# Kernel tuning notes

Measured on AMD Instinct MI355X. Metric: run time of the kernel, lower is better.

## Reference

```python
import jax, jax.numpy as jnp
import numpy as np

B, S, D_MODEL, HEADS = 4, 2048, 1024, 16
D = D_MODEL // HEADS  # 64


def setup_inputs() -> dict:
    key = jax.random.key(0)
    ks = jax.random.split(key, 12)
    s = 0.02
    return {
        "query": jax.random.normal(ks[0], (B, S, D_MODEL), jnp.float32),
        "key": jax.random.normal(ks[1], (B, S, D_MODEL), jnp.float32),
        "value": jax.random.normal(ks[2], (B, S, D_MODEL), jnp.float32),
        "mask": jnp.ones((B, 1, S, S), jnp.int32),
        "Wq": jax.random.normal(ks[3], (D, D), jnp.float32) * s,
        "bq": jnp.zeros((D,), jnp.float32),
        "Wk": jax.random.normal(ks[4], (D, D), jnp.float32) * s,
        "bk": jnp.zeros((D,), jnp.float32),
        "Wv": jax.random.normal(ks[5], (D, D), jnp.float32) * s,
        "bv": jnp.zeros((D,), jnp.float32),
        "Wo": jax.random.normal(ks[6], (D_MODEL, HEADS * D), jnp.float32) * s,
        "bo": jnp.zeros((D_MODEL,), jnp.float32),
    }


def reference(query, key, value, mask, Wq, bq, Wk, bk, Wv, bv, Wo, bo):
    b, sq, _ = query.shape
    sk = key.shape[1]
    # split heads: [B, S, H, D]
    q = query.reshape(b, sq, HEADS, D)
    k = key.reshape(b, sk, HEADS, D)
    v = value.reshape(b, sk, HEADS, D)
    # per-head linear projections (weights shared across heads), torch Linear: x @ W.T + b
    q = q @ Wq.T + bq
    k = k @ Wk.T + bk
    v = v @ Wv.T + bv
    # scores [B, H, Sq, Sk]
    score = jnp.einsum("bqhd,bkhd->bhqk", q, k)
    # NOTE: original torch code calls score.masked_fill(...) without assignment
    # (non-in-place, result discarded), so the mask has NO effect. Faithful: skip it.
    # NOTE: scaling is score / (d ** 1 / 2) == score / (d / 2), NOT score / sqrt(d).
    attn = jax.nn.softmax(score / (D / 2.0), axis=-1)
    out = jnp.einsum("bhqk,bkhd->bqhd", attn, v)
    out = out.reshape(b, sq, HEADS * D)
    return out @ Wo.T + bo
```

## Files before the change

### kernel.cpp

```cpp
#include <hip/hip_runtime.h>
#include <hip/hip_bf16.h>

#define B_   4
#define S_   2048
#define H_   16
#define D_   64
#define DM_  1024
#define BH_  (B_ * H_)

#define LOG2E_D32 0.04508422002778011f

typedef unsigned short u16;
typedef u16  u16x4  __attribute__((ext_vector_type(4)));
typedef u16  u16x8  __attribute__((ext_vector_type(8)));
typedef float f32x4 __attribute__((ext_vector_type(4)));
typedef __bf16 bf16x8 __attribute__((ext_vector_type(8)));

__device__ __forceinline__ u16 f2bf(float f) {
    __hip_bfloat16 h = __float2bfloat16(f);
    return *reinterpret_cast<u16*>(&h);
}
__device__ __forceinline__ bf16x8 cvt8(const float* p) {
    float4 a = *(const float4*)p;
    float4 b = *(const float4*)(p + 4);
    u16x8 r;
    r[0] = f2bf(a.x); r[1] = f2bf(a.y); r[2] = f2bf(a.z); r[3] = f2bf(a.w);
    r[4] = f2bf(b.x); r[5] = f2bf(b.y); r[6] = f2bf(b.z); r[7] = f2bf(b.w);
    union { u16x8 u; bf16x8 h; } cv; cv.u = r; return cv.h;
}
__device__ __forceinline__ void load_lds16(const u16* g, u16* l) {
    __builtin_amdgcn_global_load_lds(
        (const __attribute__((address_space(1))) unsigned int*)g,
        (__attribute__((address_space(3))) unsigned int*)l, 16, 0, 0);
}
#define MFMA16(a, b, c) __builtin_amdgcn_mfma_f32_16x16x32_bf16(a, b, c, 0, 0, 0)

__global__ __launch_bounds__(256) void cvt_kernel(
    const float* __restrict__ in, u16* __restrict__ outp)
{
    int i = (blockIdx.x * 256 + threadIdx.x) * 4;
    float4 v = *(const float4*)(in + i);
    u16x4 o; o[0] = f2bf(v.x); o[1] = f2bf(v.y); o[2] = f2bf(v.z); o[3] = f2bf(v.w);
    *(u16x4*)(outp + i) = o;
}

__global__ __launch_bounds__(256) void proj_kernel(
    const float* __restrict__ xq, const float* __restrict__ xk, const float* __restrict__ xv,
    const float* __restrict__ Wq, const float* __restrict__ bq,
    const float* __restrict__ Wk, const float* __restrict__ bk,
    const float* __restrict__ Wv, const float* __restrict__ bv,
    u16* __restrict__ Qp, u16* __restrict__ Kp, u16* __restrict__ Vp)
{
    __shared__ u16 vt[64 * 72];

    const int z     = blockIdx.z;
    const float* x    = (z == 0) ? xq : (z == 1) ? xk : xv;
    const float* W    = (z == 0) ? Wq : (z == 1) ? Wk : Wv;
    const float* bias = (z == 0) ? bq : (z == 1) ? bk : bv;
    const float scale = (z == 0) ? LOG2E_D32 : 1.0f;

    const int tid = threadIdx.x, w = tid >> 6, lane = tid & 63;
    const int l15 = lane & 15, quad = lane >> 4;
    const int bh = blockIdx.y, b = bh >> 4, h = bh & 15;
    const int s0 = blockIdx.x * 64;

    const int srow = s0 + w * 16 + l15;
    const float* xp = x + ((size_t)(b * S_ + srow) * H_ + h) * D_;
    bf16x8 a0 = cvt8(xp + quad * 8);
    bf16x8 a1 = cvt8(xp + 32 + quad * 8);

    f32x4 acc[4];
#pragma unroll
    for (int nt = 0; nt < 4; ++nt) {
        const float* wp = W + (nt * 16 + l15) * D_;
        f32x4 c = {0.f, 0.f, 0.f, 0.f};
        c = MFMA16(a0, cvt8(wp + quad * 8), c);
        c = MFMA16(a1, cvt8(wp + 32 + quad * 8), c);
        acc[nt] = c;
    }

    if (z < 2) {
        u16* out = (z == 0) ? Qp : Kp;
#pragma unroll
        for (int nt = 0; nt < 4; ++nt) {
            float bs = bias[nt * 16 + l15];
#pragma unroll
            for (int r = 0; r < 4; ++r) {
                int sl = w * 16 + quad * 4 + r;
                vt[sl * 72 + nt * 16 + l15] = f2bf((acc[nt][r] + bs) * scale);
            }
        }
        __syncthreads();
#pragma unroll
        for (int u = 0; u < 2; ++u) {
            int sl = (tid >> 3) + u * 32;
            int c  = tid & 7;
            u16x8 val = *(const u16x8*)&vt[sl * 72 + c * 8];
            *(u16x8*)(out + ((size_t)bh * S_ + s0 + sl) * D_ + c * 8) = val;
        }
    } else {
#pragma unroll
        for (int nt = 0; nt < 4; ++nt) {
            float bs = bias[nt * 16 + l15];
            u16x4 pu;
#pragma unroll
            for (int r = 0; r < 4; ++r) pu[r] = f2bf(acc[nt][r] + bs);
            int d  = nt * 16 + l15;
            int cc = w * 16 + quad * 4;
            int ch = (cc >> 3) ^ (d & 7);
            *(u16x4*)&vt[d * 72 + ch * 8 + (cc & 7)] = pu;
        }
        __syncthreads();
        int d  = tid >> 2;
        int cb = (tid & 3) * 16;
        size_t gbase = ((size_t)bh * 64 + d) * S_ + s0;
#pragma unroll
        for (int u = 0; u < 2; ++u) {
            int ch  = (cb >> 3) + u;
            int ch2 = ch ^ (d & 7);
            u16x8 val = *(const u16x8*)&vt[d * 72 + ch2 * 8];
            *(u16x8*)(Vp + gbase + ch * 8) = val;
        }
    }
}

__global__ __launch_bounds__(256, 3) void attn_kernel(
    const u16* __restrict__ Qp, const u16* __restrict__ Kp,
    const u16* __restrict__ Vp, u16* __restrict__ Ao)
{
    __shared__ u16 kt[2][64 * 64];
    __shared__ u16 vt[2][64 * 64];

    const int tid = threadIdx.x, w = tid >> 6, lane = tid & 63;
    const int l15 = lane & 15, quad = lane >> 4;

    const int f = blockIdx.x;
    const int xcd = f & 7, kk = f >> 3;
    const int qtile = kk & 15;
    const int bh = ((kk >> 4) << 3) | xcd;
    const int b = bh >> 4, h = bh & 15;
    const int qbase = qtile * 128 + w * 32;

    bf16x8 qf[2][2];
#pragma unroll
    for (int nt = 0; nt < 2; ++nt) {
        const bf16x8* qp = (const bf16x8*)(Qp + ((size_t)bh * S_ + qbase + nt * 16 + l15) * D_);
        qf[nt][0] = qp[quad];
        qf[nt][1] = qp[4 + quad];
    }

    f32x4 ot[4][2];
#pragma unroll
    for (int mt = 0; mt < 4; ++mt)
#pragma unroll
        for (int nt = 0; nt < 2; ++nt) ot[mt][nt] = (f32x4){0.f, 0.f, 0.f, 0.f};
    float li[2] = {0.f, 0.f};

    const size_t krow = (size_t)bh * S_;
    const size_t vrow = (size_t)bh * 64;

    const int srcA = ((quad & 1) << 5) | l15;
    const int srcB = srcA | 16;
    const bool hi  = quad >= 2;

    auto stage = [&](int it, int buf) {
        const int k0 = it * 64;
#pragma unroll
        for (int c = 0; c < 4; ++c) {
            int ci = w * 4 + c;
            if (ci < 8) {
                int chunk = ci * 64 + lane;
                int r = chunk >> 3, j = chunk & 7;
                load_lds16(Kp + (krow + k0 + r) * D_ + ((j ^ (r & 7)) << 3),
                           &kt[buf][ci * 512]);
            } else {
                int ci2 = ci - 8;
                int chunk = ci2 * 64 + lane;
                int r = chunk >> 3, j = chunk & 7;
                load_lds16(Vp + (vrow + r) * S_ + k0 + ((j ^ (r & 7)) << 3),
                           &vt[buf][ci2 * 512]);
            }
        }
    };

    stage(0, 0);

    for (int it = 0; it < S_ / 64; ++it) {
        const int p = it & 1;
        __syncthreads();

        bf16x8 ak[4][2], av[4][2];
#pragma unroll
        for (int mt = 0; mt < 4; ++mt) {
            int rk = mt * 16 + l15;
            ak[mt][0] = *(const bf16x8*)&kt[p][rk * 64 + ((quad       ^ (rk & 7)) << 3)];
            ak[mt][1] = *(const bf16x8*)&kt[p][rk * 64 + (((4 + quad) ^ (rk & 7)) << 3)];
            av[mt][0] = *(const bf16x8*)&vt[p][rk * 64 + ((quad       ^ (rk & 7)) << 3)];
            av[mt][1] = *(const bf16x8*)&vt[p][rk * 64 + (((4 + quad) ^ (rk & 7)) << 3)];
        }

        if (it + 1 < S_ / 64) stage(it + 1, p ^ 1);

        f32x4 st[4][2];
#pragma unroll
        for (int mt = 0; mt < 4; ++mt)
#pragma unroll
            for (int nt = 0; nt < 2; ++nt) {
                f32x4 c = {0.f, 0.f, 0.f, 0.f};
                c = MFMA16(ak[mt][0], qf[nt][0], c);
                c = MFMA16(ak[mt][1], qf[nt][1], c);
                st[mt][nt] = c;
            }

        uint2 pd[2][4];
#pragma unroll
        for (int nt = 0; nt < 2; ++nt) {
            float s = 0.f;
#pragma unroll
            for (int mt = 0; mt < 4; ++mt) {
                float e0 = __builtin_amdgcn_exp2f(st[mt][nt][0]);
                float e1 = __builtin_amdgcn_exp2f(st[mt][nt][1]);
                float e2 = __builtin_amdgcn_exp2f(st[mt][nt][2]);
                float e3 = __builtin_amdgcn_exp2f(st[mt][nt][3]);
                s += (e0 + e1) + (e2 + e3);
                union { u16x4 v; uint2 d; } pu;
                pu.v[0] = f2bf(e0); pu.v[1] = f2bf(e1);
                pu.v[2] = f2bf(e2); pu.v[3] = f2bf(e3);
                pd[nt][mt] = pu.d;
            }
            li[nt] += s;
        }

#pragma unroll
        for (int ks = 0; ks < 2; ++ks) {
            bf16x8 bp[2];
#pragma unroll
            for (int nt = 0; nt < 2; ++nt) {
                uint2 e0 = pd[nt][2 * ks], e1 = pd[nt][2 * ks + 1];
                int a0x = __shfl((int)e0.x, srcA), a0y = __shfl((int)e0.y, srcA);
                int a1x = __shfl((int)e1.x, srcA), a1y = __shfl((int)e1.y, srcA);
                int b0x = __shfl((int)e0.x, srcB), b0y = __shfl((int)e0.y, srcB);
                int b1x = __shfl((int)e1.x, srcB), b1y = __shfl((int)e1.y, srcB);
                union { uint4 u; bf16x8 h; } cv;
                cv.u.x = (unsigned)(hi ? a1x : a0x);
                cv.u.y = (unsigned)(hi ? a1y : a0y);
                cv.u.z = (unsigned)(hi ? b1x : b0x);
                cv.u.w = (unsigned)(hi ? b1y : b0y);
                bp[nt] = cv.h;
            }
#pragma unroll
            for (int mt = 0; mt < 4; ++mt)
#pragma unroll
                for (int nt = 0; nt < 2; ++nt)
                    ot[mt][nt] = MFMA16(av[mt][ks], bp[nt], ot[mt][nt]);
        }
    }

#pragma unroll
    for (int nt = 0; nt < 2; ++nt) {
        float l = li[nt];
        l += __shfl_xor(l, 16);
        l += __shfl_xor(l, 32);
        float inv = 1.f / l;
        int qrow = qbase + nt * 16 + l15;
        u16* orow = Ao + (((size_t)b * S_ + qrow) * H_ + h) * D_;
#pragma unroll
        for (int mt = 0; mt < 4; ++mt) {
            u16x4 o;
#pragma unroll
            for (int r = 0; r < 4; ++r) o[r] = f2bf(ot[mt][nt][r] * inv);
            *(u16x4*)(orow + mt * 16 + quad * 4) = o;
        }
    }
}

__global__ __launch_bounds__(256) void oproj_kernel(
    const u16* __restrict__ A, const u16* __restrict__ Wob,
    const float* __restrict__ bo, float* __restrict__ C)
{
    __shared__ u16 at[128 * 64];
    __shared__ u16 bt[128 * 64];

    const int tid = threadIdx.x, w = tid >> 6, lane = tid & 63;
    const int l15 = lane & 15, quad = lane >> 4;
    const int m0 = blockIdx.y * 128;
    const int n0 = blockIdx.x * 128;
    const int wm = w & 1, wn = w >> 1;

    f32x4 acc[4][4];
#pragma unroll
    for (int mt = 0; mt < 4; ++mt)
#pragma unroll
        for (int nt = 0; nt < 4; ++nt) acc[mt][nt] = (f32x4){0.f, 0.f, 0.f, 0.f};

    for (int kk = 0; kk < DM_ / 64; ++kk) {
        __syncthreads();
#pragma unroll
        for (int c = 0; c < 8; ++c) {
            int ci = w * 8 + c;
            int t  = ci & 15;
            int chunk = t * 64 + lane;
            int r = chunk >> 3, j = chunk & 7;
            int col = kk * 64 + ((j ^ (r & 7)) << 3);
            if (ci < 16) load_lds16(A   + (size_t)(m0 + r) * DM_ + col, &at[t * 512]);
            else         load_lds16(Wob + (size_t)(n0 + r) * DM_ + col, &bt[t * 512]);
        }
        __syncthreads();

#pragma unroll
        for (int ks = 0; ks < 2; ++ks) {
            bf16x8 af[4], bf[4];
#pragma unroll
            for (int mt = 0; mt < 4; ++mt) {
                int r = wm * 64 + mt * 16 + l15;
                af[mt] = *(const bf16x8*)&at[r * 64 + (((ks * 4 + quad) ^ (r & 7)) << 3)];
            }
#pragma unroll
            for (int nt = 0; nt < 4; ++nt) {
                int r = wn * 64 + nt * 16 + l15;
                bf[nt] = *(const bf16x8*)&bt[r * 64 + (((ks * 4 + quad) ^ (r & 7)) << 3)];
            }
#pragma unroll
            for (int mt = 0; mt < 4; ++mt)
#pragma unroll
                for (int nt = 0; nt < 4; ++nt)
                    acc[mt][nt] = MFMA16(af[mt], bf[nt], acc[mt][nt]);
        }
    }

#pragma unroll
    for (int nt = 0; nt < 4; ++nt) {
        int ng = n0 + wn * 64 + nt * 16 + l15;
        float bs = bo[ng];
#pragma unroll
        for (int mt = 0; mt < 4; ++mt) {
            int mg = m0 + wm * 64 + mt * 16 + quad * 4;
#pragma unroll
            for (int r = 0; r < 4; ++r)
                C[(size_t)(mg + r) * DM_ + ng] = acc[mt][nt][r] + bs;
        }
    }
}

extern "C" void kernel_launch(void* const* d_in, const int* in_sizes, int n_in,
                              void* d_out, int out_size, void* d_ws, size_t ws_size,
                              hipStream_t stream)
{
    const float* q   = (const float*)d_in[0];
    const float* k   = (const float*)d_in[1];
    const float* v   = (const float*)d_in[2];
    const float* Wq  = (const float*)d_in[4];
    const float* bq  = (const float*)d_in[5];
    const float* Wk  = (const float*)d_in[6];
    const float* bk  = (const float*)d_in[7];
    const float* Wv  = (const float*)d_in[8];
    const float* bv  = (const float*)d_in[9];
    const float* Wo  = (const float*)d_in[10];
    const float* bo  = (const float*)d_in[11];
    float* out = (float*)d_out;

    const size_t TENS = (size_t)B_ * S_ * DM_;
    u16* Qp  = (u16*)d_ws;
    u16* Kp  = Qp + TENS;
    u16* Vp  = Kp + TENS;
    u16* Ao  = Vp + TENS;
    u16* Wob = Ao + TENS;

    cvt_kernel<<<dim3((DM_ * DM_) / 1024), 256, 0, stream>>>(Wo, Wob);
    proj_kernel<<<dim3(S_ / 64, BH_, 3), 256, 0, stream>>>(
        q, k, v, Wq, bq, Wk, bk, Wv, bv, Qp, Kp, Vp);
    attn_kernel<<<dim3((S_ / 128) * BH_), 256, 0, stream>>>(Qp, Kp, Vp, Ao);
    oproj_kernel<<<dim3(DM_ / 128, (B_ * S_) / 128), 256, 0, stream>>>(Ao, Wob, bo, out);
}
```

Baseline: 367.9 us.

## Switch attention to 32x32x16 MFMA with larger per-wave query tiles

```diff
diff --git a/kernel.cpp b/kernel.cpp
--- a/kernel.cpp
+++ b/kernel.cpp
@@ -14,6 +14,7 @@
 typedef u16  u16x4  __attribute__((ext_vector_type(4)));
 typedef u16  u16x8  __attribute__((ext_vector_type(8)));
 typedef float f32x4 __attribute__((ext_vector_type(4)));
+typedef float f32x16 __attribute__((ext_vector_type(16)));
 typedef __bf16 bf16x8 __attribute__((ext_vector_type(8)));
 
 __device__ __forceinline__ u16 f2bf(float f) {
@@ -34,6 +35,7 @@
         (__attribute__((address_space(3))) unsigned int*)l, 16, 0, 0);
 }
 #define MFMA16(a, b, c) __builtin_amdgcn_mfma_f32_16x16x32_bf16(a, b, c, 0, 0, 0)
+#define MFMA32(a, b, c) __builtin_amdgcn_mfma_f32_32x32x16_bf16(a, b, c, 0, 0, 0)
 
 __global__ __launch_bounds__(256) void cvt_kernel(
     const float* __restrict__ in, u16* __restrict__ outp)
@@ -124,61 +126,56 @@
     }
 }
 
-__global__ __launch_bounds__(256, 3) void attn_kernel(
+__global__ __launch_bounds__(256, 2) void attn_kernel(
     const u16* __restrict__ Qp, const u16* __restrict__ Kp,
     const u16* __restrict__ Vp, u16* __restrict__ Ao)
 {
-    __shared__ u16 kt[2][64 * 64];
-    __shared__ u16 vt[2][64 * 64];
+    __shared__ u16 kt[2][8 * 64 * 8];
+    __shared__ u16 vt[2][8 * 64 * 8];
 
     const int tid = threadIdx.x, w = tid >> 6, lane = tid & 63;
-    const int l15 = lane & 15, quad = lane >> 4;
+    const int l31 = lane & 31, h = lane >> 5;
 
     const int f = blockIdx.x;
-    const int xcd = f & 7, kk = f >> 3;
-    const int qtile = kk & 15;
-    const int bh = ((kk >> 4) << 3) | xcd;
-    const int b = bh >> 4, h = bh & 15;
-    const int qbase = qtile * 128 + w * 32;
-
-    bf16x8 qf[2][2];
-#pragma unroll
-    for (int nt = 0; nt < 2; ++nt) {
-        const bf16x8* qp = (const bf16x8*)(Qp + ((size_t)bh * S_ + qbase + nt * 16 + l15) * D_);
-        qf[nt][0] = qp[quad];
-        qf[nt][1] = qp[4 + quad];
-    }
-
-    f32x4 ot[4][2];
-#pragma unroll
-    for (int mt = 0; mt < 4; ++mt)
-#pragma unroll
-        for (int nt = 0; nt < 2; ++nt) ot[mt][nt] = (f32x4){0.f, 0.f, 0.f, 0.f};
-    float li[2] = {0.f, 0.f};
+    const int xcd = f & 7;
+    const int g8 = f >> 3;
+    const int qtile = g8 & 7;
+    const int bh = ((g8 >> 3) << 3) | xcd;
+    const int b = bh >> 4, hh = bh & 15;
+    const int qwb = qtile * 256 + w * 64;
 
     const size_t krow = (size_t)bh * S_;
     const size_t vrow = (size_t)bh * 64;
 
-    const int srcA = ((quad & 1) << 5) | l15;
-    const int srcB = srcA | 16;
-    const bool hi  = quad >= 2;
+    bf16x8 qf[2][4];
+#pragma unroll
+    for (int nt = 0; nt < 2; ++nt)
+#pragma unroll
+        for (int kd = 0; kd < 4; ++kd)
+            qf[nt][kd] = *(const bf16x8*)(
+                Qp + ((size_t)bh * S_ + qwb + nt * 32 + l31) * D_ + kd * 16 + h * 8);
+
+    f32x16 ot[2][2];
+#pragma unroll
+    for (int dm = 0; dm < 2; ++dm)
+#pragma unroll
+        for (int nt = 0; nt < 2; ++nt)
+#pragma unroll
+            for (int r = 0; r < 16; ++r) ot[dm][nt][r] = 0.f;
+    float li[2] = {0.f, 0.f};
 
     auto stage = [&](int it, int buf) {
         const int k0 = it * 64;
 #pragma unroll
         for (int c = 0; c < 4; ++c) {
             int ci = w * 4 + c;
-            if (ci < 8) {
-                int chunk = ci * 64 + lane;
-                int r = chunk >> 3, j = chunk & 7;
-                load_lds16(Kp + (krow + k0 + r) * D_ + ((j ^ (r & 7)) << 3),
+            if (ci < 8)
+                load_lds16(Kp + (krow + k0 + lane) * D_ + ci * 8,
                            &kt[buf][ci * 512]);
-            } else {
-                int ci2 = ci - 8;
-                int chunk = ci2 * 64 + lane;
-                int r = chunk >> 3, j = chunk & 7;
-                load_lds16(Vp + (vrow + r) * S_ + k0 + ((j ^ (r & 7)) << 3),
-                           &vt[buf][ci2 * 512]);
+            else {
+                int c8 = ci - 8;
+                load_lds16(Vp + (vrow + lane) * S_ + k0 + c8 * 8,
+                           &vt[buf][c8 * 512]);
             }
         }
     };
@@ -188,89 +185,84 @@
     for (int it = 0; it < S_ / 64; ++it) {
         const int p = it & 1;
         __syncthreads();
-
-        bf16x8 ak[4][2], av[4][2];
-#pragma unroll
-        for (int mt = 0; mt < 4; ++mt) {
-            int rk = mt * 16 + l15;
-            ak[mt][0] = *(const bf16x8*)&kt[p][rk * 64 + ((quad       ^ (rk & 7)) << 3)];
-            ak[mt][1] = *(const bf16x8*)&kt[p][rk * 64 + (((4 + quad) ^ (rk & 7)) << 3)];
-            av[mt][0] = *(const bf16x8*)&vt[p][rk * 64 + ((quad       ^ (rk & 7)) << 3)];
-            av[mt][1] = *(const bf16x8*)&vt[p][rk * 64 + (((4 + quad) ^ (rk & 7)) << 3)];
-        }
-
         if (it + 1 < S_ / 64) stage(it + 1, p ^ 1);
 
-        f32x4 st[4][2];
-#pragma unroll
-        for (int mt = 0; mt < 4; ++mt)
+        f32x16 st[2][2];
+#pragma unroll
+        for (int mt = 0; mt < 2; ++mt) {
+            bf16x8 ak[4];
+#pragma unroll
+            for (int kd = 0; kd < 4; ++kd)
+                ak[kd] = *(const bf16x8*)&kt[p][((2 * kd + h) * 64 + mt * 32 + l31) * 8];
 #pragma unroll
             for (int nt = 0; nt < 2; ++nt) {
-                f32x4 c = {0.f, 0.f, 0.f, 0.f};
-                c = MFMA16(ak[mt][0], qf[nt][0], c);
-                c = MFMA16(ak[mt][1], qf[nt][1], c);
+                f32x16 c = {};
+#pragma unroll
+                for (int kd = 0; kd < 4; ++kd)
+                    c = MFMA32(ak[kd], qf[nt][kd], c);
                 st[mt][nt] = c;
             }
-
-        uint2 pd[2][4];
+        }
+
 #pragma unroll
         for (int nt = 0; nt < 2; ++nt) {
             float s = 0.f;
 #pragma unroll
-            for (int mt = 0; mt < 4; ++mt) {
-                float e0 = __builtin_amdgcn_exp2f(st[mt][nt][0]);
-                float e1 = __builtin_amdgcn_exp2f(st[mt][nt][1]);
-                float e2 = __builtin_amdgcn_exp2f(st[mt][nt][2]);
-                float e3 = __builtin_amdgcn_exp2f(st[mt][nt][3]);
-                s += (e0 + e1) + (e2 + e3);
-                union { u16x4 v; uint2 d; } pu;
-                pu.v[0] = f2bf(e0); pu.v[1] = f2bf(e1);
-                pu.v[2] = f2bf(e2); pu.v[3] = f2bf(e3);
-                pd[nt][mt] = pu.d;
-            }
+            for (int mt = 0; mt < 2; ++mt)
+#pragma unroll
+                for (int r = 0; r < 16; ++r) {
+                    float e = __builtin_amdgcn_exp2f(st[mt][nt][r]);
+                    st[mt][nt][r] = e;
+                    s += e;
+                }
             li[nt] += s;
         }
 
 #pragma unroll
-        for (int ks = 0; ks < 2; ++ks) {
-            bf16x8 bp[2];
-#pragma unroll
-            for (int nt = 0; nt < 2; ++nt) {
-                uint2 e0 = pd[nt][2 * ks], e1 = pd[nt][2 * ks + 1];
-                int a0x = __shfl((int)e0.x, srcA), a0y = __shfl((int)e0.y, srcA);
-                int a1x = __shfl((int)e1.x, srcA), a1y = __shfl((int)e1.y, srcA);
-                int b0x = __shfl((int)e0.x, srcB), b0y = __shfl((int)e0.y, srcB);
-                int b1x = __shfl((int)e1.x, srcB), b1y = __shfl((int)e1.y, srcB);
-                union { uint4 u; bf16x8 h; } cv;
-                cv.u.x = (unsigned)(hi ? a1x : a0x);
-                cv.u.y = (unsigned)(hi ? a1y : a0y);
-                cv.u.z = (unsigned)(hi ? b1x : b0x);
-                cv.u.w = (unsigned)(hi ? b1y : b0y);
-                bp[nt] = cv.h;
-            }
-#pragma unroll
-            for (int mt = 0; mt < 4; ++mt)
-#pragma unroll
-                for (int nt = 0; nt < 2; ++nt)
-                    ot[mt][nt] = MFMA16(av[mt][ks], bp[nt], ot[mt][nt]);
-        }
+        for (int mt = 0; mt < 2; ++mt)
+#pragma unroll
+            for (int s = 0; s < 2; ++s) {
+                int ks = 2 * mt + s;
+                bf16x8 av0 = *(const bf16x8*)&vt[p][((2 * ks + h) * 64 +      l31) * 8];
+                bf16x8 av1 = *(const bf16x8*)&vt[p][((2 * ks + h) * 64 + 32 + l31) * 8];
+#pragma unroll
+                for (int nt = 0; nt < 2; ++nt) {
+                    unsigned dw[4];
+#pragma unroll
+                    for (int t = 0; t < 4; ++t)
+                        dw[t] = (unsigned)f2bf(st[mt][nt][8 * s + 2 * t]) |
+                                ((unsigned)f2bf(st[mt][nt][8 * s + 2 * t + 1]) << 16);
+                    unsigned g0 = h ? dw[0] : dw[2];
+                    unsigned g1 = h ? dw[1] : dw[3];
+                    unsigned r0 = (unsigned)__shfl_xor((int)g0, 32);
+                    unsigned r1 = (unsigned)__shfl_xor((int)g1, 32);
+                    union { unsigned u[4]; bf16x8 v; } pb;
+                    pb.u[0] = h ? r0 : dw[0];
+                    pb.u[1] = h ? r1 : dw[1];
+                    pb.u[2] = h ? dw[2] : r0;
+                    pb.u[3] = h ? dw[3] : r1;
+                    ot[0][nt] = MFMA32(av0, pb.v, ot[0][nt]);
+                    ot[1][nt] = MFMA32(av1, pb.v, ot[1][nt]);
+                }
+            }
     }
 
 #pragma unroll
     for (int nt = 0; nt < 2; ++nt) {
-        float l = li[nt];
-        l += __shfl_xor(l, 16);
-        l += __shfl_xor(l, 32);
+        float l = li[nt] + __shfl_xor(li[nt], 32);
         float inv = 1.f / l;
-        int qrow = qbase + nt * 16 + l15;
-        u16* orow = Ao + (((size_t)b * S_ + qrow) * H_ + h) * D_;
-#pragma unroll
-        for (int mt = 0; mt < 4; ++mt) {
-            u16x4 o;
-#pragma unroll
-            for (int r = 0; r < 4; ++r) o[r] = f2bf(ot[mt][nt][r] * inv);
-            *(u16x4*)(orow + mt * 16 + quad * 4) = o;
-        }
+        int q = qwb + nt * 32 + l31;
+        u16* orow = Ao + ((size_t)(b * S_ + q)) * DM_ + hh * 64;
+#pragma unroll
+        for (int dm = 0; dm < 2; ++dm)
+#pragma unroll
+            for (int g = 0; g < 4; ++g) {
+                u16x4 o;
+#pragma unroll
+                for (int rr = 0; rr < 4; ++rr)
+                    o[rr] = f2bf(ot[dm][nt][4 * g + rr] * inv);
+                *(u16x4*)(orow + dm * 32 + 8 * g + 4 * h) = o;
+            }
     }
 }
 
@@ -369,6 +361,6 @@
     cvt_kernel<<<dim3((DM_ * DM_) / 1024), 256, 0, stream>>>(Wo, Wob);
     proj_kernel<<<dim3(S_ / 64, BH_, 3), 256, 0, stream>>>(
         q, k, v, Wq, bq, Wk, bk, Wv, bv, Qp, Kp, Vp);
-    attn_kernel<<<dim3((S_ / 128) * BH_), 256, 0, stream>>>(Qp, Kp, Vp, Ao);
+    attn_kernel<<<dim3(8 * 64), 256, 0, stream>>>(Qp, Kp, Vp, Ao);
     oproj_kernel<<<dim3(DM_ / 128, (B_ * S_) / 128), 256, 0, stream>>>(Ao, Wob, bo, out);
 }
```

Measured after the change: 321.4 us. 1.14x faster.
